# Kernel optimization log

Hardware: AMD Instinct MI355X
Metric: run time of the kernel (lower is better)

## Reference

```python
import jax, jax.numpy as jnp
import numpy as np

T, B, D, H = 1024, 32, 256, 256


def _gru_scan(gi, whh, bhh, h0, reverse):
    # gi: (T, B, 3H) precomputed input projections; torch GRUCell gate order r,z,n
    def step(h, gi_t):
        gh = h @ whh.T + bhh
        ir, iz, inn = jnp.split(gi_t, 3, axis=-1)
        hr, hz, hn = jnp.split(gh, 3, axis=-1)
        r = jax.nn.sigmoid(ir + hr)
        z = jax.nn.sigmoid(iz + hz)
        n = jnp.tanh(inn + r * hn)
        h_new = (1.0 - z) * n + z * h
        return h_new, h_new
    _, ys = jax.lax.scan(step, h0, gi, reverse=reverse)
    return ys  # (T, B, H)


def _roll_seq(seq, shifts):
    # per-example roll along the time axis; seq: (T, B, *), shifts: (B,)
    return jax.vmap(lambda s, k: jnp.roll(s, k, axis=0), in_axes=(1, 0), out_axes=1)(seq, shifts)


def _layer(x, lengths, wih_f, whh_f, bih_f, bhh_f, wih_b, whh_b, bih_b, bhh_b):
    Tt, Bb = x.shape[0], x.shape[1]
    h0 = jnp.zeros((Bb, whh_f.shape[-1]), x.dtype)
    batch_ix = jnp.arange(Bb)
    # forward direction: scan over padded input (padding steps run too, as in torch code)
    gi_f = jnp.einsum('tbd,gd->tbg', x, wih_f) + bih_f
    ys_f = _gru_scan(gi_f, whh_f, bhh_f, h0, reverse=False)
    hn_f = ys_f[lengths - 1, batch_ix]  # state at last valid step
    # backward direction: align_sequence(shift_right=True) moves valid data to the end,
    # then a reversed scan; output is rolled back (shift left) afterwards.
    x_sh = _roll_seq(x, Tt - lengths)
    gi_b = jnp.einsum('tbd,gd->tbg', x_sh, wih_b) + bih_b
    ys_b = _gru_scan(gi_b, whh_b, bhh_b, h0, reverse=True)
    hn_b = ys_b[Tt - lengths, batch_ix]  # state after processing `length` reversed steps
    ys_b = _roll_seq(ys_b, -(Tt - lengths))
    # interleave dirs like torch.stack(dim=2).view(T, B, -1) -> concat [fwd, bwd]
    out = jnp.concatenate([ys_f[:, :, None, :], ys_b[:, :, None, :]], axis=2).reshape(Tt, Bb, -1)
    return out, hn_f, hn_b


def setup_inputs() -> dict:
    key = jax.random.key(0)
    ks = jax.random.split(key, 20)
    scale = 1.0 / np.sqrt(H)
    u = lambda k, shape: jax.random.uniform(k, shape, jnp.float32, -scale, scale)
    inp = {'x': jax.random.normal(ks[0], (T, B, D), jnp.float32)}
    i = 1
    for layer, in_dim in [('l0', D), ('l1', 2 * H)]:
        for d in ('f', 'b'):
            inp[f'w_ih_{layer}{d}'] = u(ks[i], (3 * H, in_dim)); i += 1
            inp[f'w_hh_{layer}{d}'] = u(ks[i], (3 * H, H)); i += 1
            inp[f'b_ih_{layer}{d}'] = u(ks[i], (3 * H,)); i += 1
            inp[f'b_hh_{layer}{d}'] = u(ks[i], (3 * H,)); i += 1
    lengths = jax.random.randint(ks[17], (B,), T // 2, T + 1)
    lengths = jnp.sort(lengths)[::-1].at[0].set(T).astype(jnp.int32)  # descending, max == T
    inp['lengths'] = lengths
    return inp


def reference(x,
              w_ih_l0f, w_hh_l0f, b_ih_l0f, b_hh_l0f,
              w_ih_l0b, w_hh_l0b, b_ih_l0b, b_hh_l0b,
              w_ih_l1f, w_hh_l1f, b_ih_l1f, b_hh_l1f,
              w_ih_l1b, w_hh_l1b, b_ih_l1b, b_hh_l1b,
              lengths):
    out0, h0f, h0b = _layer(x, lengths,
                            w_ih_l0f, w_hh_l0f, b_ih_l0f, b_hh_l0f,
                            w_ih_l0b, w_hh_l0b, b_ih_l0b, b_hh_l0b)
    # no inter-layer dropout (eval / dropout=0); layer output fed unmasked, as in torch code
    out1, h1f, h1b = _layer(out0, lengths,
                            w_ih_l1f, w_hh_l1f, b_ih_l1f, b_hh_l1f,
                            w_ih_l1b, w_hh_l1b, b_ih_l1b, b_hh_l1b)
    last_hidden = jnp.stack([h0f, h0b, h1f, h1b], axis=0)  # (L*2, B, H)
    indicator = (jnp.arange(out1.shape[0])[:, None] < lengths[None, :])[..., None]
    output = out1 * indicator.astype(out1.dtype)
    return output, last_hidden
```

## Files before the change

### kernel.cpp

```cpp
#include <hip/hip_runtime.h>
#include <hip/hip_bf16.h>
#include <hip/hip_fp16.h>

#define T_ 1024
#define B_ 32
#define H_ 256
#define G3 768

typedef _Float16 half2_t __attribute__((ext_vector_type(2)));

__device__ __forceinline__ float sigmoidf_(float x) { return 1.f / (1.f + __expf(-x)); }
__device__ __forceinline__ float tanhf_(float x) {
    float e = __expf(2.f * x);
    return (e - 1.f) / (e + 1.f);
}

__device__ __forceinline__ void sync_lds() {
    asm volatile("s_waitcnt lgkmcnt(0)" ::: "memory");
    asm volatile("s_barrier" ::: "memory");
}

__device__ __forceinline__ float fdot2_(unsigned int w, unsigned int h, float acc) {
#if __has_builtin(__builtin_amdgcn_fdot2)
    return __builtin_amdgcn_fdot2(__builtin_bit_cast(half2_t, w),
                                  __builtin_bit_cast(half2_t, h), acc, false);
#else
    half2_t a = __builtin_bit_cast(half2_t, w);
    half2_t b = __builtin_bit_cast(half2_t, h);
    return acc + (float)a[0] * (float)b[0] + (float)a[1] * (float)b[1];
#endif
}

__device__ __forceinline__ unsigned int pack_f16rn(float x, float y) {
    unsigned short ux = __half_as_ushort(__float2half_rn(x));
    unsigned short uy = __half_as_ushort(__float2half_rn(y));
    return (unsigned int)ux | ((unsigned int)uy << 16);
}

template <typename CT>
__global__ __launch_bounds__(256) void gemm_bias_nt(
    const float* __restrict__ A, const float* __restrict__ W,
    const float* __restrict__ bias, CT* __restrict__ C,
    int M, int N, int K)
{
    __shared__ float As[16][68];
    __shared__ float Ws[16][68];
    const int tid = threadIdx.x;
    const int bm = blockIdx.y * 64;
    const int bn = blockIdx.x * 64;
    const int lr = tid & 63;
    const int lc = tid >> 6;
    const int tx = tid & 15;
    const int ty = tid >> 4;

    const float* Ap = A + (size_t)(bm + lr) * K + lc * 4;
    const float* Wp = W + (size_t)(bn + lr) * K + lc * 4;

    float acc[4][4];
#pragma unroll
    for (int i = 0; i < 4; ++i)
#pragma unroll
        for (int j = 0; j < 4; ++j) acc[i][j] = 0.f;

    for (int k0 = 0; k0 < K; k0 += 16) {
        float4 av = *(const float4*)(Ap + k0);
        float4 wv = *(const float4*)(Wp + k0);
        __syncthreads();
        As[lc * 4 + 0][lr] = av.x; As[lc * 4 + 1][lr] = av.y;
        As[lc * 4 + 2][lr] = av.z; As[lc * 4 + 3][lr] = av.w;
        Ws[lc * 4 + 0][lr] = wv.x; Ws[lc * 4 + 1][lr] = wv.y;
        Ws[lc * 4 + 2][lr] = wv.z; Ws[lc * 4 + 3][lr] = wv.w;
        __syncthreads();
#pragma unroll
        for (int kk = 0; kk < 16; ++kk) {
            float4 a4 = *(const float4*)&As[kk][ty * 4];
            float4 w4 = *(const float4*)&Ws[kk][tx * 4];
            float am[4] = {a4.x, a4.y, a4.z, a4.w};
            float wn[4] = {w4.x, w4.y, w4.z, w4.w};
#pragma unroll
            for (int i = 0; i < 4; ++i)
#pragma unroll
                for (int j = 0; j < 4; ++j) acc[i][j] += am[i] * wn[j];
        }
    }

#pragma unroll
    for (int i = 0; i < 4; ++i) {
        size_t cbase = (size_t)(bm + ty * 4 + i) * N + bn + tx * 4;
#pragma unroll
        for (int j = 0; j < 4; ++j) {
            float v = acc[i][j] + bias[bn + tx * 4 + j];
            C[cbase + j] = (CT)v;
        }
    }
}

template <typename PT>
__global__ __launch_bounds__(512, 2) void gru_scan_shfl(
    const PT* __restrict__ Pf, const PT* __restrict__ Pb,
    const float* __restrict__ Wf, const float* __restrict__ Wb,
    const float* __restrict__ bhf, const float* __restrict__ bhb,
    const int* __restrict__ lengths,
    float* __restrict__ out,
    float* __restrict__ hn,
    int do_mask)
{
    const int b = blockIdx.x >> 1;
    const int dir = blockIdx.x & 1;
    const PT* P = dir ? Pb : Pf;
    const float* W = dir ? Wb : Wf;
    const float* bh = dir ? bhb : bhf;
    const int len = lengths[b];

    __shared__ __align__(16) unsigned short h16[2][H_];

    const int tid = threadIdx.x;
    const int lane = tid & 63;
    const int wave = tid >> 6;
    const int j = wave * 32 + (lane & 31);
    const int kh = lane >> 5;

    unsigned int wr[64], wz[64], wn[64];
    {
        const float4* r0 = (const float4*)(W + (size_t)j * H_ + kh * 128);
        const float4* r1 = (const float4*)(W + (size_t)(j + 256) * H_ + kh * 128);
        const float4* r2 = (const float4*)(W + (size_t)(j + 512) * H_ + kh * 128);
#pragma unroll
        for (int q = 0; q < 32; ++q) {
            float4 a = r0[q]; wr[2 * q] = pack_f16rn(a.x, a.y); wr[2 * q + 1] = pack_f16rn(a.z, a.w);
            float4 c = r1[q]; wz[2 * q] = pack_f16rn(c.x, c.y); wz[2 * q + 1] = pack_f16rn(c.z, c.w);
            float4 d = r2[q]; wn[2 * q] = pack_f16rn(d.x, d.y); wn[2 * q + 1] = pack_f16rn(d.z, d.w);
            __builtin_amdgcn_sched_barrier(0);
        }
    }

    const float bh0 = bh[j];
    const float bh1 = bh[j + 256];
    const float bh2 = bh[j + 512];

    float hreg = 0.f;
    if (tid < H_) h16[0][tid] = 0;

    float* outp = out + (size_t)b * 512 + dir * 256;
    float* hnp = hn + (size_t)dir * (B_ * H_) + (size_t)b * H_;

    int crow = dir ? ((len - 1) & (T_ - 1)) : 0;
    int prow = dir ? ((len - 2) & (T_ - 1)) : 1;
    const int rstep = dir ? -1 : 1;
    const PT* Pbase = P + (size_t)b * G3 + j;

    float cir, ciz, cin;
    {
        const PT* pp = Pbase + (size_t)crow * (B_ * G3);
        cir = (float)pp[0]; ciz = (float)pp[256]; cin = (float)pp[512];
    }
    sync_lds();

#pragma unroll 1
    for (int s = 0; s < T_; ++s) {
        float nir = 0.f, niz = 0.f, nin = 0.f;
        if (s + 1 < T_) {
            const PT* pp = Pbase + (size_t)prow * (B_ * G3);
            nir = (float)pp[0]; niz = (float)pp[256]; nin = (float)pp[512];
        }

        float ar0 = 0.f, ar1 = 0.f, az0 = 0.f, az1 = 0.f, an0 = 0.f, an1 = 0.f;
        const uint4* hv = ((const uint4*)h16[s & 1]) + kh * 16;
#pragma unroll
        for (int m = 0; m < 8; ++m) {
            uint4 ua = hv[2 * m];
            uint4 ub = hv[2 * m + 1];
            ar0 = fdot2_(wr[8 * m + 0], ua.x, ar0);
            az0 = fdot2_(wz[8 * m + 0], ua.x, az0);
            an0 = fdot2_(wn[8 * m + 0], ua.x, an0);
            ar1 = fdot2_(wr[8 * m + 1], ua.y, ar1);
            az1 = fdot2_(wz[8 * m + 1], ua.y, az1);
            an1 = fdot2_(wn[8 * m + 1], ua.y, an1);
            ar0 = fdot2_(wr[8 * m + 2], ua.z, ar0);
            az0 = fdot2_(wz[8 * m + 2], ua.z, az0);
            an0 = fdot2_(wn[8 * m + 2], ua.z, an0);
            ar1 = fdot2_(wr[8 * m + 3], ua.w, ar1);
            az1 = fdot2_(wz[8 * m + 3], ua.w, az1);
            an1 = fdot2_(wn[8 * m + 3], ua.w, an1);
            ar0 = fdot2_(wr[8 * m + 4], ub.x, ar0);
            az0 = fdot2_(wz[8 * m + 4], ub.x, az0);
            an0 = fdot2_(wn[8 * m + 4], ub.x, an0);
            ar1 = fdot2_(wr[8 * m + 5], ub.y, ar1);
            az1 = fdot2_(wz[8 * m + 5], ub.y, az1);
            an1 = fdot2_(wn[8 * m + 5], ub.y, an1);
            ar0 = fdot2_(wr[8 * m + 6], ub.z, ar0);
            az0 = fdot2_(wz[8 * m + 6], ub.z, az0);
            an0 = fdot2_(wn[8 * m + 6], ub.z, an0);
            ar1 = fdot2_(wr[8 * m + 7], ub.w, ar1);
            az1 = fdot2_(wz[8 * m + 7], ub.w, az1);
            an1 = fdot2_(wn[8 * m + 7], ub.w, an1);
            if (m & 1) __builtin_amdgcn_sched_barrier(0);
        }
        float ar = ar0 + ar1;
        float az = az0 + az1;
        float an = an0 + an1;
        ar += __shfl_xor(ar, 32);
        az += __shfl_xor(az, 32);
        an += __shfl_xor(an, 32);

        float r = sigmoidf_(cir + ar + bh0);
        float z = sigmoidf_(ciz + az + bh1);
        float nn = tanhf_(cin + r * (an + bh2));
        float hnew = (1.f - z) * nn + z * hreg;
        hreg = hnew;

        if (lane < 32) {
            h16[(s & 1) ^ 1][j] = __half_as_ushort(__float2half_rn(hnew));
            float ov = (do_mask && crow >= len) ? 0.f : hnew;
            outp[(size_t)crow * (B_ * 512) + j] = ov;
            if (s == len - 1) hnp[j] = hnew;
        }
        sync_lds();

        cir = nir; ciz = niz; cin = nin;
        crow = (crow + rstep) & (T_ - 1);
        prow = (prow + rstep) & (T_ - 1);
    }
}

extern "C" void kernel_launch(void* const* d_in, const int* in_sizes, int n_in,
                              void* d_out, int out_size, void* d_ws, size_t ws_size,
                              hipStream_t stream)
{
    const float* x        = (const float*)d_in[0];
    const float* w_ih_l0f = (const float*)d_in[1];
    const float* w_hh_l0f = (const float*)d_in[2];
    const float* b_ih_l0f = (const float*)d_in[3];
    const float* b_hh_l0f = (const float*)d_in[4];
    const float* w_ih_l0b = (const float*)d_in[5];
    const float* w_hh_l0b = (const float*)d_in[6];
    const float* b_ih_l0b = (const float*)d_in[7];
    const float* b_hh_l0b = (const float*)d_in[8];
    const float* w_ih_l1f = (const float*)d_in[9];
    const float* w_hh_l1f = (const float*)d_in[10];
    const float* b_ih_l1f = (const float*)d_in[11];
    const float* b_hh_l1f = (const float*)d_in[12];
    const float* w_ih_l1b = (const float*)d_in[13];
    const float* w_hh_l1b = (const float*)d_in[14];
    const float* b_ih_l1b = (const float*)d_in[15];
    const float* b_hh_l1b = (const float*)d_in[16];
    const int*   lengths  = (const int*)d_in[17];

    float* out = (float*)d_out;
    const size_t OUT_OFF = (size_t)T_ * B_ * 512;
    float* hn0 = out + OUT_OFF;
    float* hn1 = hn0 + 2 * B_ * H_;

    const size_t PE = (size_t)T_ * B_ * G3;
    const int M = T_ * B_;
    dim3 gg(G3 / 64, M / 64);

    if (ws_size >= 2 * PE * sizeof(float)) {
        float* P0 = (float*)d_ws;
        float* P1 = P0 + PE;
        gemm_bias_nt<float><<<gg, 256, 0, stream>>>(x, w_ih_l0f, b_ih_l0f, P0, M, G3, 256);
        gemm_bias_nt<float><<<gg, 256, 0, stream>>>(x, w_ih_l0b, b_ih_l0b, P1, M, G3, 256);
        gru_scan_shfl<float><<<64, 512, 0, stream>>>(P0, P1, w_hh_l0f, w_hh_l0b,
                                                     b_hh_l0f, b_hh_l0b, lengths, out, hn0, 0);
        gemm_bias_nt<float><<<gg, 256, 0, stream>>>(out, w_ih_l1f, b_ih_l1f, P0, M, G3, 512);
        gemm_bias_nt<float><<<gg, 256, 0, stream>>>(out, w_ih_l1b, b_ih_l1b, P1, M, G3, 512);
        gru_scan_shfl<float><<<64, 512, 0, stream>>>(P0, P1, w_hh_l1f, w_hh_l1b,
                                                     b_hh_l1f, b_hh_l1b, lengths, out, hn1, 1);
    } else if (ws_size >= 2 * PE * sizeof(__hip_bfloat16)) {
        __hip_bfloat16* P0 = (__hip_bfloat16*)d_ws;
        __hip_bfloat16* P1 = P0 + PE;
        gemm_bias_nt<__hip_bfloat16><<<gg, 256, 0, stream>>>(x, w_ih_l0f, b_ih_l0f, P0, M, G3, 256);
        gemm_bias_nt<__hip_bfloat16><<<gg, 256, 0, stream>>>(x, w_ih_l0b, b_ih_l0b, P1, M, G3, 256);
        gru_scan_shfl<__hip_bfloat16><<<64, 512, 0, stream>>>(P0, P1, w_hh_l0f, w_hh_l0b,
                                                              b_hh_l0f, b_hh_l0b, lengths, out, hn0, 0);
        gemm_bias_nt<__hip_bfloat16><<<gg, 256, 0, stream>>>(out, w_ih_l1f, b_ih_l1f, P0, M, G3, 512);
        gemm_bias_nt<__hip_bfloat16><<<gg, 256, 0, stream>>>(out, w_ih_l1b, b_ih_l1b, P1, M, G3, 512);
        gru_scan_shfl<__hip_bfloat16><<<64, 512, 0, stream>>>(P0, P1, w_hh_l1f, w_hh_l1b,
                                                              b_hh_l1f, b_hh_l1b, lengths, out, hn1, 1);
    }
}
```

Baseline: 3.676 ms.

## Split GRU recurrence K-dimension four ways across 1024-thread blocks with padded LDS

The recurrent scan now uses 1024 threads per block. Each output unit's dot product is split across four lane groups, each holding 64 K-elements of weights in registers instead of 128, and the partial sums are combined with two xor shuffles. The hidden-state LDS buffer is padded to 72-element strides, apparently to avoid bank conflicts between the quarter groups. The fdot2 builtin is replaced by inline v_dot2_f32_f16 asm. The aim is to halve per-thread serial work and register pressure on the latency-bound step, at the cost of an extra shuffle round and a 1024-thread barrier every step.

After: 4.649 ms. 26.5% more time.

```diff
diff --git a/kernel.cpp b/kernel.cpp
--- a/kernel.cpp
+++ b/kernel.cpp
@@ -7,8 +7,6 @@
 #define H_ 256
 #define G3 768
 
-typedef _Float16 half2_t __attribute__((ext_vector_type(2)));
-
 __device__ __forceinline__ float sigmoidf_(float x) { return 1.f / (1.f + __expf(-x)); }
 __device__ __forceinline__ float tanhf_(float x) {
     float e = __expf(2.f * x);
@@ -20,21 +18,14 @@
     asm volatile("s_barrier" ::: "memory");
 }
 
-__device__ __forceinline__ float fdot2_(unsigned int w, unsigned int h, float acc) {
-#if __has_builtin(__builtin_amdgcn_fdot2)
-    return __builtin_amdgcn_fdot2(__builtin_bit_cast(half2_t, w),
-                                  __builtin_bit_cast(half2_t, h), acc, false);
-#else
-    half2_t a = __builtin_bit_cast(half2_t, w);
-    half2_t b = __builtin_bit_cast(half2_t, h);
-    return acc + (float)a[0] * (float)b[0] + (float)a[1] * (float)b[1];
-#endif
-}
-
-__device__ __forceinline__ unsigned int pack_f16rn(float x, float y) {
+__device__ __forceinline__ void dot2a(float& acc, unsigned w, unsigned h) {
+    asm("v_dot2_f32_f16 %0, %1, %2, %0" : "+v"(acc) : "v"(w), "v"(h));
+}
+
+__device__ __forceinline__ unsigned pack_f16rn(float x, float y) {
     unsigned short ux = __half_as_ushort(__float2half_rn(x));
     unsigned short uy = __half_as_ushort(__float2half_rn(y));
-    return (unsigned int)ux | ((unsigned int)uy << 16);
+    return (unsigned)ux | ((unsigned)uy << 16);
 }
 
 template <typename CT>
@@ -96,7 +87,7 @@
 }
 
 template <typename PT>
-__global__ __launch_bounds__(512, 2) void gru_scan_shfl(
+__global__ __launch_bounds__(1024, 4) void gru_scan_q(
     const PT* __restrict__ Pf, const PT* __restrict__ Pb,
     const float* __restrict__ Wf, const float* __restrict__ Wb,
     const float* __restrict__ bhf, const float* __restrict__ bhb,
@@ -112,21 +103,20 @@
     const float* bh = dir ? bhb : bhf;
     const int len = lengths[b];
 
-    __shared__ __align__(16) unsigned short h16[2][H_];
+    __shared__ __align__(16) unsigned short h16[2][288];
 
     const int tid = threadIdx.x;
     const int lane = tid & 63;
-    const int wave = tid >> 6;
-    const int j = wave * 32 + (lane & 31);
-    const int kh = lane >> 5;
-
-    unsigned int wr[64], wz[64], wn[64];
+    const int j = (tid >> 6) * 16 + (lane & 15);
+    const int kq = lane >> 4;
+
+    unsigned wr[32], wz[32], wn[32];
     {
-        const float4* r0 = (const float4*)(W + (size_t)j * H_ + kh * 128);
-        const float4* r1 = (const float4*)(W + (size_t)(j + 256) * H_ + kh * 128);
-        const float4* r2 = (const float4*)(W + (size_t)(j + 512) * H_ + kh * 128);
-#pragma unroll
-        for (int q = 0; q < 32; ++q) {
+        const float4* r0 = (const float4*)(W + (size_t)j * H_ + kq * 64);
+        const float4* r1 = (const float4*)(W + (size_t)(j + 256) * H_ + kq * 64);
+        const float4* r2 = (const float4*)(W + (size_t)(j + 512) * H_ + kq * 64);
+#pragma unroll
+        for (int q = 0; q < 16; ++q) {
             float4 a = r0[q]; wr[2 * q] = pack_f16rn(a.x, a.y); wr[2 * q + 1] = pack_f16rn(a.z, a.w);
             float4 c = r1[q]; wz[2 * q] = pack_f16rn(c.x, c.y); wz[2 * q + 1] = pack_f16rn(c.z, c.w);
             float4 d = r2[q]; wn[2 * q] = pack_f16rn(d.x, d.y); wn[2 * q + 1] = pack_f16rn(d.z, d.w);
@@ -139,7 +129,7 @@
     const float bh2 = bh[j + 512];
 
     float hreg = 0.f;
-    if (tid < H_) h16[0][tid] = 0;
+    if (tid < 288) h16[0][tid] = 0;
 
     float* outp = out + (size_t)b * 512 + dir * 256;
     float* hnp = hn + (size_t)dir * (B_ * H_) + (size_t)b * H_;
@@ -158,59 +148,45 @@
 
 #pragma unroll 1
     for (int s = 0; s < T_; ++s) {
-        float nir = 0.f, niz = 0.f, nin = 0.f;
-        if (s + 1 < T_) {
+        float nir, niz, nin;
+        {
             const PT* pp = Pbase + (size_t)prow * (B_ * G3);
             nir = (float)pp[0]; niz = (float)pp[256]; nin = (float)pp[512];
         }
 
-        float ar0 = 0.f, ar1 = 0.f, az0 = 0.f, az1 = 0.f, an0 = 0.f, an1 = 0.f;
-        const uint4* hv = ((const uint4*)h16[s & 1]) + kh * 16;
+        float ar0 = 0.f, az0 = 0.f, an0 = 0.f;
+        float ar1 = 0.f, az1 = 0.f, an1 = 0.f;
+        const uint4* hv = (const uint4*)(&h16[s & 1][kq * 72]);
 #pragma unroll
         for (int m = 0; m < 8; ++m) {
-            uint4 ua = hv[2 * m];
-            uint4 ub = hv[2 * m + 1];
-            ar0 = fdot2_(wr[8 * m + 0], ua.x, ar0);
-            az0 = fdot2_(wz[8 * m + 0], ua.x, az0);
-            an0 = fdot2_(wn[8 * m + 0], ua.x, an0);
-            ar1 = fdot2_(wr[8 * m + 1], ua.y, ar1);
-            az1 = fdot2_(wz[8 * m + 1], ua.y, az1);
-            an1 = fdot2_(wn[8 * m + 1], ua.y, an1);
-            ar0 = fdot2_(wr[8 * m + 2], ua.z, ar0);
-            az0 = fdot2_(wz[8 * m + 2], ua.z, az0);
-            an0 = fdot2_(wn[8 * m + 2], ua.z, an0);
-            ar1 = fdot2_(wr[8 * m + 3], ua.w, ar1);
-            az1 = fdot2_(wz[8 * m + 3], ua.w, az1);
-            an1 = fdot2_(wn[8 * m + 3], ua.w, an1);
-            ar0 = fdot2_(wr[8 * m + 4], ub.x, ar0);
-            az0 = fdot2_(wz[8 * m + 4], ub.x, az0);
-            an0 = fdot2_(wn[8 * m + 4], ub.x, an0);
-            ar1 = fdot2_(wr[8 * m + 5], ub.y, ar1);
-            az1 = fdot2_(wz[8 * m + 5], ub.y, az1);
-            an1 = fdot2_(wn[8 * m + 5], ub.y, an1);
-            ar0 = fdot2_(wr[8 * m + 6], ub.z, ar0);
-            az0 = fdot2_(wz[8 * m + 6], ub.z, az0);
-            an0 = fdot2_(wn[8 * m + 6], ub.z, an0);
-            ar1 = fdot2_(wr[8 * m + 7], ub.w, ar1);
-            az1 = fdot2_(wz[8 * m + 7], ub.w, az1);
-            an1 = fdot2_(wn[8 * m + 7], ub.w, an1);
-            if (m & 1) __builtin_amdgcn_sched_barrier(0);
+            uint4 u = hv[m];
+            if (m & 1) {
+                dot2a(ar1, wr[4 * m + 0], u.x); dot2a(az1, wz[4 * m + 0], u.x); dot2a(an1, wn[4 * m + 0], u.x);
+                dot2a(ar1, wr[4 * m + 1], u.y); dot2a(az1, wz[4 * m + 1], u.y); dot2a(an1, wn[4 * m + 1], u.y);
+                dot2a(ar1, wr[4 * m + 2], u.z); dot2a(az1, wz[4 * m + 2], u.z); dot2a(an1, wn[4 * m + 2], u.z);
+                dot2a(ar1, wr[4 * m + 3], u.w); dot2a(az1, wz[4 * m + 3], u.w); dot2a(an1, wn[4 * m + 3], u.w);
+            } else {
+                dot2a(ar0, wr[4 * m + 0], u.x); dot2a(az0, wz[4 * m + 0], u.x); dot2a(an0, wn[4 * m + 0], u.x);
+                dot2a(ar0, wr[4 * m + 1], u.y); dot2a(az0, wz[4 * m + 1], u.y); dot2a(an0, wn[4 * m + 1], u.y);
+                dot2a(ar0, wr[4 * m + 2], u.z); dot2a(az0, wz[4 * m + 2], u.z); dot2a(an0, wn[4 * m + 2], u.z);
+                dot2a(ar0, wr[4 * m + 3], u.w); dot2a(az0, wz[4 * m + 3], u.w); dot2a(an0, wn[4 * m + 3], u.w);
+            }
+            __builtin_amdgcn_sched_barrier(0);
         }
         float ar = ar0 + ar1;
         float az = az0 + az1;
         float an = an0 + an1;
-        ar += __shfl_xor(ar, 32);
-        az += __shfl_xor(az, 32);
-        an += __shfl_xor(an, 32);
+        ar += __shfl_xor(ar, 16); az += __shfl_xor(az, 16); an += __shfl_xor(an, 16);
+        ar += __shfl_xor(ar, 32); az += __shfl_xor(az, 32); an += __shfl_xor(an, 32);
 
         float r = sigmoidf_(cir + ar + bh0);
         float z = sigmoidf_(ciz + az + bh1);
-        float nn = tanhf_(cin + r * (an + bh2));
-        float hnew = (1.f - z) * nn + z * hreg;
+        float nng = tanhf_(cin + r * (an + bh2));
+        float hnew = (1.f - z) * nng + z * hreg;
         hreg = hnew;
 
-        if (lane < 32) {
-            h16[(s & 1) ^ 1][j] = __half_as_ushort(__float2half_rn(hnew));
+        if (kq == 0) {
+            h16[(s & 1) ^ 1][(j >> 6) * 72 + (j & 63)] = __half_as_ushort(__float2half_rn(hnew));
             float ov = (do_mask && crow >= len) ? 0.f : hnew;
             outp[(size_t)crow * (B_ * 512) + j] = ov;
             if (s == len - 1) hnp[j] = hnew;
@@ -260,22 +236,22 @@
         float* P1 = P0 + PE;
         gemm_bias_nt<float><<<gg, 256, 0, stream>>>(x, w_ih_l0f, b_ih_l0f, P0, M, G3, 256);
         gemm_bias_nt<float><<<gg, 256, 0, stream>>>(x, w_ih_l0b, b_ih_l0b, P1, M, G3, 256);
-        gru_scan_shfl<float><<<64, 512, 0, stream>>>(P0, P1, w_hh_l0f, w_hh_l0b,
-                                                     b_hh_l0f, b_hh_l0b, lengths, out, hn0, 0);
+        gru_scan_q<float><<<64, 1024, 0, stream>>>(P0, P1, w_hh_l0f, w_hh_l0b,
+                                                   b_hh_l0f, b_hh_l0b, lengths, out, hn0, 0);
         gemm_bias_nt<float><<<gg, 256, 0, stream>>>(out, w_ih_l1f, b_ih_l1f, P0, M, G3, 512);
         gemm_bias_nt<float><<<gg, 256, 0, stream>>>(out, w_ih_l1b, b_ih_l1b, P1, M, G3, 512);
-        gru_scan_shfl<float><<<64, 512, 0, stream>>>(P0, P1, w_hh_l1f, w_hh_l1b,
-                                                     b_hh_l1f, b_hh_l1b, lengths, out, hn1, 1);
+        gru_scan_q<float><<<64, 1024, 0, stream>>>(P0, P1, w_hh_l1f, w_hh_l1b,
+                                                   b_hh_l1f, b_hh_l1b, lengths, out, hn1, 1);
     } else if (ws_size >= 2 * PE * sizeof(__hip_bfloat16)) {
         __hip_bfloat16* P0 = (__hip_bfloat16*)d_ws;
         __hip_bfloat16* P1 = P0 + PE;
         gemm_bias_nt<__hip_bfloat16><<<gg, 256, 0, stream>>>(x, w_ih_l0f, b_ih_l0f, P0, M, G3, 256);
         gemm_bias_nt<__hip_bfloat16><<<gg, 256, 0, stream>>>(x, w_ih_l0b, b_ih_l0b, P1, M, G3, 256);
-        gru_scan_shfl<__hip_bfloat16><<<64, 512, 0, stream>>>(P0, P1, w_hh_l0f, w_hh_l0b,
-                                                              b_hh_l0f, b_hh_l0b, lengths, out, hn0, 0);
+        gru_scan_q<__hip_bfloat16><<<64, 1024, 0, stream>>>(P0, P1, w_hh_l0f, w_hh_l0b,
+                                                            b_hh_l0f, b_hh_l0b, lengths, out, hn0, 0);
         gemm_bias_nt<__hip_bfloat16><<<gg, 256, 0, stream>>>(out, w_ih_l1f, b_ih_l1f, P0, M, G3, 512);
         gemm_bias_nt<__hip_bfloat16><<<gg, 256, 0, stream>>>(out, w_ih_l1b, b_ih_l1b, P1, M, G3, 512);
-        gru_scan_shfl<__hip_bfloat16><<<64, 512, 0, stream>>>(P0, P1, w_hh_l1f, w_hh_l1b,
-                                                              b_hh_l1f, b_hh_l1b, lengths, out, hn1, 1);
-    }
-}
+        gru_scan_q<__hip_bfloat16><<<64, 1024, 0, stream>>>(P0, P1, w_hh_l1f, w_hh_l1b,
+                                                            b_hh_l1f, b_hh_l1b, lengths, out, hn1, 1);
+    }
+}
```
